# Kernel optimization log

Measured on AMD Instinct MI355X. Metric: run time of the kernel, lower is better.

## Reference

```python
import jax, jax.numpy as jnp
import numpy as np

B, S, D, H, P = 4, 512, 512, 8, 16
DK = D // H  # 64


def setup_inputs() -> dict:
    k0 = jax.random.key(0)
    ks = jax.random.split(k0, 10)
    std = 0.02
    lin = lambda k, shape: jax.random.normal(k, shape, dtype=jnp.float32) * std
    inp = {}
    inp["query"] = jax.random.normal(ks[0], (B, S, D), dtype=jnp.float32)
    inp["key"] = jax.random.normal(ks[1], (B, S, D), dtype=jnp.float32)
    inp["value"] = jax.random.normal(ks[2], (B, S, D), dtype=jnp.float32)
    inp["Wq"] = lin(ks[3], (D, D)); inp["bq"] = jnp.zeros((D,), jnp.float32)
    inp["Wk"] = lin(ks[4], (D, D)); inp["bk"] = jnp.zeros((D,), jnp.float32)
    inp["Wv"] = lin(ks[5], (D, D)); inp["bv"] = jnp.zeros((D,), jnp.float32)
    inp["Wo"] = lin(ks[6], (D, D)); inp["bo"] = jnp.zeros((D,), jnp.float32)
    inp["rel_table"] = lin(ks[7], (2 * P + 1, DK))  # nn.Embedding(2P+1, d_k)
    inp["gamma"] = jnp.ones((D,), jnp.float32)
    inp["beta"] = jnp.zeros((D,), jnp.float32)
    inp["mask"] = jnp.ones((B, S), dtype=jnp.int32)
    inp["relative_positions"] = jax.random.randint(ks[8], (B, S, S, DK), -32, 33, dtype=jnp.int32)
    return inp


def reference(query, key, value, Wq, bq, Wk, bk, Wv, bv, Wo, bo, rel_table, gamma, beta, mask, relative_positions):
    b, s, d = query.shape
    dk = rel_table.shape[1]
    h = d // dk
    pmax = (rel_table.shape[0] - 1) // 2

    def heads(x, W, bias):
        return (x @ W.T + bias).reshape(b, s, h, dk).transpose(0, 2, 1, 3)  # [b,h,s,dk]

    Q = heads(query, Wq, bq)
    K = heads(key, Wk, bk)
    V = heads(value, Wv, bv)

    scores = jnp.einsum('bhid,bhjd->bhij', Q, K) / jnp.sqrt(jnp.float32(dk))

    # torch: einsum('bhid,bijde->bhije', Q, emb(idx)).mean(-1)
    # mean over e commutes with the d-contraction -> pre-average the table.
    idx = jnp.clip(relative_positions, -pmax, pmax) + pmax  # [b,i,j,d]
    bias_d = rel_table.mean(axis=-1)[idx]                   # [b,i,j,d]
    scores = scores + jnp.einsum('bhid,bijd->bhij', Q, bias_d)

    scores = jnp.where(mask[:, None, None, :] == 0, jnp.float32(-1e9), scores)
    attn = jax.nn.softmax(scores, axis=-1)  # dropout is identity in eval

    ctx = jnp.einsum('bhij,bhjd->bhid', attn, V).transpose(0, 2, 1, 3).reshape(b, s, d)
    out = ctx @ Wo.T + bo

    x = out + query  # residual
    mu = x.mean(-1, keepdims=True)
    var = x.var(-1, keepdims=True)
    y = (x - mu) / jnp.sqrt(var + 1e-5) * gamma + beta
    return (y, attn)
```

## Files before the change

### kernel.cpp

```cpp
#include <hip/hip_runtime.h>
#include <hip/hip_bf16.h>

#define BB 4
#define SS 512
#define DD 512
#define HH 8
#define DK 64
#define PP 16
#define TSZ 33

typedef __bf16 bf16x8 __attribute__((ext_vector_type(8)));
typedef __bf16 bf16x4 __attribute__((ext_vector_type(4)));
typedef float  f32x4  __attribute__((ext_vector_type(4)));

__device__ inline bf16x8 cvt8(const float* __restrict__ p) {
    f32x4 a = *(const f32x4*)p;
    f32x4 b = *(const f32x4*)(p + 4);
    bf16x8 r;
    r[0] = (__bf16)a[0]; r[1] = (__bf16)a[1]; r[2] = (__bf16)a[2]; r[3] = (__bf16)a[3];
    r[4] = (__bf16)b[0]; r[5] = (__bf16)b[1]; r[6] = (__bf16)b[2]; r[7] = (__bf16)b[3];
    return r;
}

__global__ void tmean_kernel(const float* __restrict__ rel_table, float* __restrict__ Tm) {
    int t = threadIdx.x;
    if (t < TSZ) {
        float s = 0.f;
        for (int e = 0; e < DK; ++e) s += rel_table[t * DK + e];
        Tm[t] = s * (1.f / DK);
    }
}

__global__ void proj_mfma_kernel(const float* __restrict__ X0, const float* __restrict__ X1,
                                 const float* __restrict__ X2,
                                 const float* __restrict__ W0, const float* __restrict__ W1,
                                 const float* __restrict__ W2,
                                 const float* __restrict__ B0, const float* __restrict__ B1,
                                 const float* __restrict__ B2,
                                 __bf16* __restrict__ O0, __bf16* __restrict__ O1,
                                 __bf16* __restrict__ O2) {
    int z = blockIdx.z;
    const float* X = (z == 0) ? X0 : (z == 1) ? X1 : X2;
    const float* W = (z == 0) ? W0 : (z == 1) ? W1 : W2;
    const float* bias = (z == 0) ? B0 : (z == 1) ? B1 : B2;
    __bf16* out = (z == 0) ? O0 : (z == 1) ? O1 : O2;
    int mode = (z == 2);

    int lane = threadIdx.x, wave = threadIdx.y;
    int tm = blockIdx.y * 4 + wave;
    int tn = blockIdx.x;
    int m = lane & 15, quad = lane >> 4;

    const float* arow = X + (size_t)(tm * 16 + m) * DD + quad * 8;
    const float* brow = W + (size_t)(tn * 16 + m) * DD + quad * 8;

    f32x4 acc = {0.f, 0.f, 0.f, 0.f};
    for (int k0 = 0; k0 < DD; k0 += 32) {
        bf16x8 a = cvt8(arow + k0);
        bf16x8 b = cvt8(brow + k0);
        acc = __builtin_amdgcn_mfma_f32_16x16x32_bf16(a, b, acc, 0, 0, 0);
    }

    int col = tn * 16 + m;
    int h = col >> 6, dk = col & (DK - 1);
    float bv = bias[col];
#pragma unroll
    for (int r = 0; r < 4; ++r) {
        int rowg = tm * 16 + quad * 4 + r;
        int b = rowg >> 9, i = rowg & (SS - 1);
        float v = acc[r] + bv;
        if (mode == 0)
            out[((size_t)(b * HH + h) * SS + i) * DK + dk] = (__bf16)v;
        else
            out[((size_t)(b * HH + h) * DK + dk) * SS + i] = (__bf16)v;
    }
}

__launch_bounds__(512, 2)
__global__ void f1_kernel(const __bf16* __restrict__ Qbf, const __bf16* __restrict__ Kbf,
                          const int* __restrict__ relpos, const float* __restrict__ Tm,
                          const int* __restrict__ mask, float* __restrict__ attn,
                          float* __restrict__ pm, float* __restrict__ pl) {
    __shared__ __bf16 tm_sh[16 * 16 * 72];
    __shared__ __bf16 qs_sh[8 * 17 * 72];
    __shared__ float  bias_sh[8 * 16 * 17];
    __shared__ float  tmean_sh[TSZ];

    int l = threadIdx.x, w = threadIdx.y;
    int t = w * 64 + l;
    int jq = blockIdx.x, i0 = blockIdx.y, b = blockIdx.z;

    if (t < TSZ) tmean_sh[t] = Tm[t];

    {
        int f = t * 16;
        int h = f >> 10, i = (f >> 6) & 15, d0 = f & 63;
        const __bf16* src = Qbf + ((size_t)(b * HH + h) * SS + i0 * 16 + i) * DK + d0;
        bf16x8 v0 = *(const bf16x8*)src;
        bf16x8 v1 = *(const bf16x8*)(src + 8);
        *(bf16x8*)&qs_sh[(h * 17 + i) * 72 + d0] = v0;
        *(bf16x8*)&qs_sh[(h * 17 + i) * 72 + d0 + 8] = v1;
    }

    int m = l & 15, quad = l >> 4;
    const __bf16* qrow = Qbf + ((size_t)(b * HH + w) * SS + i0 * 16 + m) * DK + quad * 8;
    bf16x8 a0 = *(const bf16x8*)qrow;
    bf16x8 a1 = *(const bf16x8*)(qrow + 32);

    f32x4 acc[8];
#pragma unroll
    for (int jt = 0; jt < 8; ++jt) {
        const __bf16* krow = Kbf + ((size_t)(b * HH + w) * SS + jq * 128 + jt * 16 + m) * DK + quad * 8;
        bf16x8 b0 = *(const bf16x8*)krow;
        bf16x8 b1 = *(const bf16x8*)(krow + 32);
        f32x4 c = {0.f, 0.f, 0.f, 0.f};
        c = __builtin_amdgcn_mfma_f32_16x16x32_bf16(a0, b0, c, 0, 0, 0);
        c = __builtin_amdgcn_mfma_f32_16x16x32_bf16(a1, b1, c, 0, 0, 0);
        acc[jt] = c;
    }

    int h8 = l & 7, j8 = l >> 3;

    for (int jt = 0; jt < 8; ++jt) {
        __syncthreads();
        const int* gidx = relpos + ((size_t)(b * SS + i0 * 16) * SS + jq * 128 + jt * 16) * DK;
#pragma unroll
        for (int c = 0; c < 8; ++c) {
            int f = c * 2048 + t * 4;
            int i = f >> 10, rem = f & 1023;
            int4 v = *(const int4*)(gidx + (size_t)i * (SS * DK) + rem);
            int j = rem >> 6, d = rem & 63;
            int c0 = min(max(v.x, -PP), PP) + PP;
            int c1 = min(max(v.y, -PP), PP) + PP;
            int c2 = min(max(v.z, -PP), PP) + PP;
            int c3 = min(max(v.w, -PP), PP) + PP;
            bf16x4 pk = {(__bf16)tmean_sh[c0], (__bf16)tmean_sh[c1],
                         (__bf16)tmean_sh[c2], (__bf16)tmean_sh[c3]};
            *(bf16x4*)&tm_sh[(i * 16 + j) * 72 + d] = pk;
        }
        __syncthreads();
#pragma unroll
        for (int ii = 0; ii < 2; ++ii) {
            int i = w * 2 + ii;
#pragma unroll
            for (int half = 0; half < 2; ++half) {
                int j = j8 + 8 * half;
                float bacc = 0.f;
#pragma unroll
                for (int d8 = 0; d8 < 8; ++d8) {
                    bf16x8 tv = *(bf16x8*)&tm_sh[(i * 16 + j) * 72 + d8 * 8];
                    bf16x8 qv = *(bf16x8*)&qs_sh[(h8 * 17 + i) * 72 + d8 * 8];
#pragma unroll
                    for (int k = 0; k < 8; ++k) bacc += (float)tv[k] * (float)qv[k];
                }
                bias_sh[(h8 * 16 + i) * 17 + j] = bacc;
            }
        }
        __syncthreads();
#pragma unroll
        for (int r = 0; r < 4; ++r)
            acc[jt][r] = acc[jt][r] * 0.125f + bias_sh[(w * 16 + quad * 4 + r) * 17 + m];
    }

#pragma unroll
    for (int jt = 0; jt < 8; ++jt) {
        int mv = mask[b * SS + jq * 128 + jt * 16 + m];
        if (mv == 0) {
#pragma unroll
            for (int r = 0; r < 4; ++r) acc[jt][r] = -1e9f;
        }
    }

#pragma unroll
    for (int r = 0; r < 4; ++r) {
        float mx = -1e30f;
#pragma unroll
        for (int jt = 0; jt < 8; ++jt) mx = fmaxf(mx, acc[jt][r]);
        mx = fmaxf(mx, __shfl_xor(mx, 1));
        mx = fmaxf(mx, __shfl_xor(mx, 2));
        mx = fmaxf(mx, __shfl_xor(mx, 4));
        mx = fmaxf(mx, __shfl_xor(mx, 8));
        float sum = 0.f;
#pragma unroll
        for (int jt = 0; jt < 8; ++jt) {
            float e = __expf(acc[jt][r] - mx);
            acc[jt][r] = e;
            sum += e;
        }
        sum += __shfl_xor(sum, 1);
        sum += __shfl_xor(sum, 2);
        sum += __shfl_xor(sum, 4);
        sum += __shfl_xor(sum, 8);
        if (m == 0) {
            int row = i0 * 16 + quad * 4 + r;
            pm[((size_t)(b * HH + w) * SS + row) * 4 + jq] = mx;
            pl[((size_t)(b * HH + w) * SS + row) * 4 + jq] = sum;
        }
    }

#pragma unroll
    for (int jt = 0; jt < 8; ++jt) {
#pragma unroll
        for (int r = 0; r < 4; ++r) {
            attn[((size_t)(b * HH + w) * SS + i0 * 16 + quad * 4 + r) * SS
                 + jq * 128 + jt * 16 + m] = acc[jt][r];
        }
    }
}

__launch_bounds__(256, 4)
__global__ void f2_kernel(float* __restrict__ attn, const float* __restrict__ pm,
                          const float* __restrict__ pl, const __bf16* __restrict__ Vt,
                          __bf16* __restrict__ ctx_bsd) {
    __shared__ float scl[4][16];
    __shared__ __bf16 p_sh[16 * 520];

    int t = threadIdx.x;
    int l = t & 63, wv = t >> 6;
    int i0 = blockIdx.x, bh = blockIdx.y;

    if (t < 16) {
        int row = i0 * 16 + t;
        float m0 = pm[((size_t)bh * SS + row) * 4 + 0];
        float m1 = pm[((size_t)bh * SS + row) * 4 + 1];
        float m2 = pm[((size_t)bh * SS + row) * 4 + 2];
        float m3 = pm[((size_t)bh * SS + row) * 4 + 3];
        float l0 = pl[((size_t)bh * SS + row) * 4 + 0];
        float l1 = pl[((size_t)bh * SS + row) * 4 + 1];
        float l2 = pl[((size_t)bh * SS + row) * 4 + 2];
        float l3 = pl[((size_t)bh * SS + row) * 4 + 3];
        float M = fmaxf(fmaxf(m0, m1), fmaxf(m2, m3));
        float e0 = __expf(m0 - M), e1 = __expf(m1 - M);
        float e2 = __expf(m2 - M), e3 = __expf(m3 - M);
        float L = l0 * e0 + l1 * e1 + l2 * e2 + l3 * e3;
        float inv = 1.f / L;
        scl[0][t] = e0 * inv; scl[1][t] = e1 * inv;
        scl[2][t] = e2 * inv; scl[3][t] = e3 * inv;
    }
    __syncthreads();

    float* arow = attn + ((size_t)bh * SS + i0 * 16) * SS;
#pragma unroll
    for (int rr = 0; rr < 4; ++rr) {
        int row = wv * 4 + rr;
#pragma unroll
        for (int it = 0; it < 2; ++it) {
            int col = it * 256 + l * 4;
            f32x4 v = *(f32x4*)(arow + (size_t)row * SS + col);
            float s = scl[col >> 7][row];
            v[0] *= s; v[1] *= s; v[2] *= s; v[3] *= s;
            *(f32x4*)(arow + (size_t)row * SS + col) = v;
            bf16x4 pk = {(__bf16)v[0], (__bf16)v[1], (__bf16)v[2], (__bf16)v[3]};
            *(bf16x4*)&p_sh[row * 520 + col] = pk;
        }
    }
    __syncthreads();

    int m = l & 15, quad = l >> 4;
    f32x4 acc = {0.f, 0.f, 0.f, 0.f};
    const __bf16* vrow = Vt + ((size_t)bh * DK + wv * 16 + m) * SS + quad * 8;
    for (int k0 = 0; k0 < SS; k0 += 32) {
        bf16x8 aF = *(bf16x8*)&p_sh[m * 520 + k0 + quad * 8];
        bf16x8 bF = *(const bf16x8*)(vrow + k0);
        acc = __builtin_amdgcn_mfma_f32_16x16x32_bf16(aF, bF, acc, 0, 0, 0);
    }
    int b = bh >> 3, h = bh & 7;
#pragma unroll
    for (int r = 0; r < 4; ++r) {
        ctx_bsd[((size_t)(b * SS + i0 * 16 + quad * 4 + r)) * DD + h * DK + wv * 16 + m]
            = (__bf16)acc[r];
    }
}

__global__ void outproj_mfma_kernel(const __bf16* __restrict__ Xc, const float* __restrict__ Wo,
                                    const float* __restrict__ bo, const float* __restrict__ query,
                                    float* __restrict__ xres) {
    int lane = threadIdx.x, wave = threadIdx.y;
    int tm = blockIdx.y * 4 + wave;
    int tn = blockIdx.x;
    int m = lane & 15, quad = lane >> 4;

    const __bf16* arow = Xc + (size_t)(tm * 16 + m) * DD + quad * 8;
    const float*  brow = Wo + (size_t)(tn * 16 + m) * DD + quad * 8;

    f32x4 acc = {0.f, 0.f, 0.f, 0.f};
    for (int k0 = 0; k0 < DD; k0 += 32) {
        bf16x8 a = *(const bf16x8*)(arow + k0);
        bf16x8 b = cvt8(brow + k0);
        acc = __builtin_amdgcn_mfma_f32_16x16x32_bf16(a, b, acc, 0, 0, 0);
    }

    int col = tn * 16 + m;
    float bv = bo[col];
#pragma unroll
    for (int r = 0; r < 4; ++r) {
        int rowg = tm * 16 + quad * 4 + r;
        xres[(size_t)rowg * DD + col] = acc[r] + bv + query[(size_t)rowg * DD + col];
    }
}

__global__ void ln_kernel(const float* __restrict__ x, const float* __restrict__ gamma,
                          const float* __restrict__ beta, float* __restrict__ y) {
    int r = blockIdx.x;
    int t = threadIdx.x;
    float v0 = x[r * DD + t];
    float v1 = x[r * DD + t + 256];
    __shared__ float red[4];
    float s = v0 + v1;
#pragma unroll
    for (int off = 32; off >= 1; off >>= 1) s += __shfl_xor(s, off);
    if ((t & 63) == 0) red[t >> 6] = s;
    __syncthreads();
    float mu = (red[0] + red[1] + red[2] + red[3]) * (1.f / DD);
    __syncthreads();
    float d0 = v0 - mu, d1 = v1 - mu;
    float sq = d0 * d0 + d1 * d1;
#pragma unroll
    for (int off = 32; off >= 1; off >>= 1) sq += __shfl_xor(sq, off);
    if ((t & 63) == 0) red[t >> 6] = sq;
    __syncthreads();
    float var = (red[0] + red[1] + red[2] + red[3]) * (1.f / DD);
    float inv = rsqrtf(var + 1e-5f);
    y[r * DD + t] = d0 * inv * gamma[t] + beta[t];
    y[r * DD + t + 256] = d1 * inv * gamma[t + 256] + beta[t + 256];
}

extern "C" void kernel_launch(void* const* d_in, const int* in_sizes, int n_in,
                              void* d_out, int out_size, void* d_ws, size_t ws_size,
                              hipStream_t stream) {
    const float* query  = (const float*)d_in[0];
    const float* key    = (const float*)d_in[1];
    const float* value  = (const float*)d_in[2];
    const float* Wq     = (const float*)d_in[3];
    const float* bq     = (const float*)d_in[4];
    const float* Wk     = (const float*)d_in[5];
    const float* bk     = (const float*)d_in[6];
    const float* Wv     = (const float*)d_in[7];
    const float* bv     = (const float*)d_in[8];
    const float* Wo     = (const float*)d_in[9];
    const float* bo     = (const float*)d_in[10];
    const float* rtab   = (const float*)d_in[11];
    const float* gamma  = (const float*)d_in[12];
    const float* beta   = (const float*)d_in[13];
    const int*   mask   = (const int*)d_in[14];
    const int*   relpos = (const int*)d_in[15];

    float* out = (float*)d_out;
    float* y    = out;
    float* attn = out + (size_t)BB * SS * DD;

    char* wsb = (char*)d_ws;
    float*  Tm    = (float*)wsb;   wsb += 256;
    __bf16* Qbf   = (__bf16*)wsb;  wsb += (size_t)BB * HH * SS * DK * 2;
    __bf16* Kbf   = (__bf16*)wsb;  wsb += (size_t)BB * HH * SS * DK * 2;
    __bf16* Vtbf  = (__bf16*)wsb;  wsb += (size_t)BB * HH * DK * SS * 2;
    __bf16* ctxbf = (__bf16*)wsb;  wsb += (size_t)BB * SS * DD * 2;
    float*  xres  = (float*)wsb;   wsb += (size_t)BB * SS * DD * 4;
    float*  pm    = (float*)wsb;   wsb += (size_t)BB * HH * SS * 4 * 4;
    float*  pl    = (float*)wsb;   wsb += (size_t)BB * HH * SS * 4 * 4;

    hipLaunchKernelGGL(tmean_kernel, dim3(1), dim3(64), 0, stream, rtab, Tm);

    dim3 wblk(64, 4);
    hipLaunchKernelGGL(proj_mfma_kernel, dim3(DD / 16, (BB * SS) / 64, 3), wblk, 0, stream,
                       query, key, value, Wq, Wk, Wv, bq, bk, bv, Qbf, Kbf, Vtbf);

    hipLaunchKernelGGL(f1_kernel, dim3(4, SS / 16, BB), dim3(64, 8), 0, stream,
                       Qbf, Kbf, relpos, Tm, mask, attn, pm, pl);

    hipLaunchKernelGGL(f2_kernel, dim3(SS / 16, BB * HH), dim3(256), 0, stream,
                       attn, pm, pl, Vtbf, ctxbf);

    hipLaunchKernelGGL(outproj_mfma_kernel, dim3(DD / 16, (BB * SS) / 64), wblk, 0, stream,
                       ctxbf, Wo, bo, query, xres);

    hipLaunchKernelGGL(ln_kernel, dim3(BB * SS), dim3(256), 0, stream, xres, gamma, beta, y);
}
```

Baseline: 581.5 us.

## Compute relative-position bias with MFMA and register LUT instead of LDS staging

Replaces the shared-memory staging of the gathered table values and the scalar dot products with a per-wave MFMA. Each lane loads its relpos indices into registers, looks up the averaged table through ds_bpermute from a per-lane register, packs the results into bf16 fragments, and multiplies them against Q rows. Relpos loads for the next row are prefetched while the current row computes, and the per-jt barriers are replaced by one barrier. In exchange the bias buffer in shared memory becomes larger and half of the MFMA output rows are computed and then discarded.

```diff
diff --git a/kernel.cpp b/kernel.cpp
--- a/kernel.cpp
+++ b/kernel.cpp
@@ -12,6 +12,8 @@
 typedef __bf16 bf16x8 __attribute__((ext_vector_type(8)));
 typedef __bf16 bf16x4 __attribute__((ext_vector_type(4)));
 typedef float  f32x4  __attribute__((ext_vector_type(4)));
+
+union U8 { bf16x8 v; int u[4]; };
 
 __device__ inline bf16x8 cvt8(const float* __restrict__ p) {
     f32x4 a = *(const f32x4*)p;
@@ -81,28 +83,59 @@
                           const int* __restrict__ relpos, const float* __restrict__ Tm,
                           const int* __restrict__ mask, float* __restrict__ attn,
                           float* __restrict__ pm, float* __restrict__ pl) {
-    __shared__ __bf16 tm_sh[16 * 16 * 72];
-    __shared__ __bf16 qs_sh[8 * 17 * 72];
-    __shared__ float  bias_sh[8 * 16 * 17];
-    __shared__ float  tmean_sh[TSZ];
+    __shared__ float bias_sh[8 * 16 * 132];
 
     int l = threadIdx.x, w = threadIdx.y;
-    int t = w * 64 + l;
     int jq = blockIdx.x, i0 = blockIdx.y, b = blockIdx.z;
-
-    if (t < TSZ) tmean_sh[t] = Tm[t];
+    int m = l & 15, quad = l >> 4;
+
+    float tmf = Tm[l < TSZ ? l : 0];
+    int tmb = (int)__builtin_bit_cast(unsigned short, (__bf16)tmf);
 
     {
-        int f = t * 16;
-        int h = f >> 10, i = (f >> 6) & 15, d0 = f & 63;
-        const __bf16* src = Qbf + ((size_t)(b * HH + h) * SS + i0 * 16 + i) * DK + d0;
-        bf16x8 v0 = *(const bf16x8*)src;
-        bf16x8 v1 = *(const bf16x8*)(src + 8);
-        *(bf16x8*)&qs_sh[(h * 17 + i) * 72 + d0] = v0;
-        *(bf16x8*)&qs_sh[(h * 17 + i) * 72 + d0 + 8] = v1;
-    }
-
-    int m = l & 15, quad = l >> 4;
+        const int ISTR = SS * DK;
+        const int* rbase = relpos + ((size_t)(b * SS + i0 * 16) * SS + jq * 128 + w * 16 + m) * DK + quad * 8;
+        int4 u0 = *(const int4*)(rbase);
+        int4 u1 = *(const int4*)(rbase + 4);
+        int4 u2 = *(const int4*)(rbase + 32);
+        int4 u3 = *(const int4*)(rbase + 36);
+        for (int i = 0; i < 16; ++i) {
+            int4 n0, n1, n2, n3;
+            if (i < 15) {
+                const int* nb = rbase + (i + 1) * ISTR;
+                n0 = *(const int4*)(nb);
+                n1 = *(const int4*)(nb + 4);
+                n2 = *(const int4*)(nb + 32);
+                n3 = *(const int4*)(nb + 36);
+            }
+            const __bf16* qp = Qbf + ((size_t)(b * HH + (m & 7)) * SS + i0 * 16 + i) * DK + quad * 8;
+            bf16x8 A0 = *(const bf16x8*)qp;
+            bf16x8 A1 = *(const bf16x8*)(qp + 32);
+#define LUT(vv) __builtin_amdgcn_ds_bpermute((min(max((vv), -PP), PP) + PP) << 2, tmb)
+            U8 Bf0, Bf1;
+            Bf0.u[0] = LUT(u0.x) | (LUT(u0.y) << 16);
+            Bf0.u[1] = LUT(u0.z) | (LUT(u0.w) << 16);
+            Bf0.u[2] = LUT(u1.x) | (LUT(u1.y) << 16);
+            Bf0.u[3] = LUT(u1.z) | (LUT(u1.w) << 16);
+            Bf1.u[0] = LUT(u2.x) | (LUT(u2.y) << 16);
+            Bf1.u[1] = LUT(u2.z) | (LUT(u2.w) << 16);
+            Bf1.u[2] = LUT(u3.x) | (LUT(u3.y) << 16);
+            Bf1.u[3] = LUT(u3.z) | (LUT(u3.w) << 16);
+#undef LUT
+            f32x4 accB = {0.f, 0.f, 0.f, 0.f};
+            accB = __builtin_amdgcn_mfma_f32_16x16x32_bf16(A0, Bf0.v, accB, 0, 0, 0);
+            accB = __builtin_amdgcn_mfma_f32_16x16x32_bf16(A1, Bf1.v, accB, 0, 0, 0);
+            if (quad < 2) {
+#pragma unroll
+                for (int r = 0; r < 4; ++r) {
+                    int h = quad * 4 + r;
+                    bias_sh[h * 2112 + i * 132 + w * 16 + m] = accB[r];
+                }
+            }
+            u0 = n0; u1 = n1; u2 = n2; u3 = n3;
+        }
+    }
+
     const __bf16* qrow = Qbf + ((size_t)(b * HH + w) * SS + i0 * 16 + m) * DK + quad * 8;
     bf16x8 a0 = *(const bf16x8*)qrow;
     bf16x8 a1 = *(const bf16x8*)(qrow + 32);
@@ -119,47 +152,15 @@
         acc[jt] = c;
     }
 
-    int h8 = l & 7, j8 = l >> 3;
-
+    __syncthreads();
+
+#pragma unroll
     for (int jt = 0; jt < 8; ++jt) {
-        __syncthreads();
-        const int* gidx = relpos + ((size_t)(b * SS + i0 * 16) * SS + jq * 128 + jt * 16) * DK;
-#pragma unroll
-        for (int c = 0; c < 8; ++c) {
-            int f = c * 2048 + t * 4;
-            int i = f >> 10, rem = f & 1023;
-            int4 v = *(const int4*)(gidx + (size_t)i * (SS * DK) + rem);
-            int j = rem >> 6, d = rem & 63;
-            int c0 = min(max(v.x, -PP), PP) + PP;
-            int c1 = min(max(v.y, -PP), PP) + PP;
-            int c2 = min(max(v.z, -PP), PP) + PP;
-            int c3 = min(max(v.w, -PP), PP) + PP;
-            bf16x4 pk = {(__bf16)tmean_sh[c0], (__bf16)tmean_sh[c1],
-                         (__bf16)tmean_sh[c2], (__bf16)tmean_sh[c3]};
-            *(bf16x4*)&tm_sh[(i * 16 + j) * 72 + d] = pk;
-        }
-        __syncthreads();
-#pragma unroll
-        for (int ii = 0; ii < 2; ++ii) {
-            int i = w * 2 + ii;
-#pragma unroll
-            for (int half = 0; half < 2; ++half) {
-                int j = j8 + 8 * half;
-                float bacc = 0.f;
-#pragma unroll
-                for (int d8 = 0; d8 < 8; ++d8) {
-                    bf16x8 tv = *(bf16x8*)&tm_sh[(i * 16 + j) * 72 + d8 * 8];
-                    bf16x8 qv = *(bf16x8*)&qs_sh[(h8 * 17 + i) * 72 + d8 * 8];
-#pragma unroll
-                    for (int k = 0; k < 8; ++k) bacc += (float)tv[k] * (float)qv[k];
-                }
-                bias_sh[(h8 * 16 + i) * 17 + j] = bacc;
-            }
-        }
-        __syncthreads();
-#pragma unroll
-        for (int r = 0; r < 4; ++r)
-            acc[jt][r] = acc[jt][r] * 0.125f + bias_sh[(w * 16 + quad * 4 + r) * 17 + m];
+#pragma unroll
+        for (int r = 0; r < 4; ++r) {
+            float bv = bias_sh[w * 2112 + (quad * 4 + r) * 132 + jt * 16 + m];
+            acc[jt][r] = acc[jt][r] * 0.125f + bv;
+        }
     }
 
 #pragma unroll
```

Result: faster. 538.8 us (-7.3%).
